# Performance work log

Measured on AMD Instinct MI355X. Metric: run time of the kernel, lower is better.

The kernel has to match this reference:

```python
import jax, jax.numpy as jnp
import numpy as np

B, T, D = 128, 2048, 256


def setup_inputs() -> dict:
    key = jax.random.key(0)
    ks = jax.random.split(key, 6)
    s = 1.0 / np.sqrt(D)  # kaiming-uniform-ish scale for bias-free Linear
    return {
        "x": jax.random.normal(ks[0], (B, T, D), jnp.float32),
        "W_in": jax.random.normal(ks[1], (D, D), jnp.float32) * s,
        "W_select": jax.random.normal(ks[2], (D, D), jnp.float32) * s,
        "W_gate": jax.random.normal(ks[3], (D, D), jnp.float32) * s,
        "W_out": jax.random.normal(ks[4], (D, D), jnp.float32) * s,
        "W_delta": jax.random.normal(ks[5], (D, D), jnp.float32) * s,
        "log_a": jnp.zeros((D,), jnp.float32),  # module inits log_a = zeros
    }


def _diag_recurrence(decay, update):
    # state_t = decay_t * state_{t-1} + update_t, state_{-1} = 0 (zero-init fast path)
    # First-order linear recurrence as an associative scan:
    # (a1,b1) o (a2,b2) = (a1*a2, a2*b1 + b2)
    def combine(c1, c2):
        a1, b1 = c1
        a2, b2 = c2
        return a1 * a2, a2 * b1 + b2

    _, states = jax.lax.associative_scan(combine, (decay, update), axis=1)
    return states  # (B, T, D)


def reference(x, W_in, W_select, W_gate, W_out, W_delta, log_a):
    # selective diag-SSM (a_mode='diag'):
    #   delta  = softplus(delta_proj(x))                  timestep / selectivity
    #   decay  = exp(-delta * exp(log_a))                 in (0, 1]
    #   update = delta * sigmoid(select_proj(x)) * in_proj(x)
    #   states = scan(state = decay*state + update)
    #   y      = states * silu(gate_proj(x)); out = out_proj(y)
    delta = jax.nn.softplus(jnp.einsum("btd,ed->bte", x, W_delta))
    decay = jnp.exp(-delta * jnp.exp(log_a))
    u = jnp.einsum("btd,ed->bte", x, W_in)
    sel = jax.nn.sigmoid(jnp.einsum("btd,ed->bte", x, W_select))
    update = delta * sel * u
    states = _diag_recurrence(decay, update)
    gate = jax.nn.silu(jnp.einsum("btd,ed->bte", x, W_gate))
    return jnp.einsum("btd,ed->bte", states * gate, W_out)
```

## Files before the change

### kernel.cpp

```cpp
#include <hip/hip_runtime.h>
#include <hip/hip_bf16.h>
#include <hip/hip_fp16.h>
#include <math.h>


typedef __attribute__((ext_vector_type(8))) short s16x8;
typedef __attribute__((ext_vector_type(4))) float f32x4;
typedef __attribute__((ext_vector_type(4))) unsigned short u16x4;

#define D_DIM 256
#define T_DIM 2048
#define B_DIM 128
#define NCHUNK 16
#define CLEN 128
#define BK 64

__device__ __forceinline__ unsigned short f2bf(float f) {
    union { float f; unsigned int u; } v; v.f = f;
    unsigned int r = v.u + 0x7fffu + ((v.u >> 16) & 1u);
    return (unsigned short)(r >> 16);
}
__device__ __forceinline__ float bf2f(unsigned short s) {
    union { unsigned int u; float f; } v; v.u = ((unsigned int)s) << 16;
    return v.f;
}
__device__ __forceinline__ void gload_lds16(const void* g, void* l) {
    __builtin_amdgcn_global_load_lds(
        (const __attribute__((address_space(1))) unsigned int*)g,
        (__attribute__((address_space(3))) unsigned int*)l, 16, 0, 0);
}

__global__ __launch_bounds__(256) void prep_kernel(
    const float* __restrict__ W_in, const float* __restrict__ W_select,
    const float* __restrict__ W_gate, const float* __restrict__ W_out,
    const float* __restrict__ W_delta, const float* __restrict__ log_a,
    unsigned short* __restrict__ Wb, float* __restrict__ ea)
{
    int i = blockIdx.x * 256 + threadIdx.x;
    if (i < 4 * 65536) {
        int row = i >> 8, k = i & 255;
        int n = row >> 2, w = row & 3;
        const float* src = (w == 0) ? W_delta : (w == 1) ? W_select
                         : (w == 2) ? W_in    : W_gate;
        Wb[i] = f2bf(src[n * 256 + k]);
    } else if (i < 5 * 65536) {
        Wb[i] = f2bf(W_out[i - 4 * 65536]);
    } else if (i < 5 * 65536 + 256) {
        int j = i - 5 * 65536;
        ea[j] = expf(log_a[j]);
    }
}

__global__ __launch_bounds__(256) void xcast_kernel(
    const float* __restrict__ x, unsigned short* __restrict__ xb)
{
    size_t i = ((size_t)blockIdx.x * 256 + threadIdx.x) * 8;
    float4 p0 = *(const float4*)(x + i);
    float4 p1 = *(const float4*)(x + i + 4);
    s16x8 a;
    a[0] = (short)f2bf(p0.x); a[1] = (short)f2bf(p0.y);
    a[2] = (short)f2bf(p0.z); a[3] = (short)f2bf(p0.w);
    a[4] = (short)f2bf(p1.x); a[5] = (short)f2bf(p1.y);
    a[6] = (short)f2bf(p1.z); a[7] = (short)f2bf(p1.w);
    *(s16x8*)(xb + i) = a;
}

__global__ __launch_bounds__(256, 3) void gemm_fused_kernel(
    const unsigned short* __restrict__ xb, const unsigned short* __restrict__ Wcat,
    const float* __restrict__ ea,
    __half2* __restrict__ du, unsigned short* __restrict__ gate)
{
    __shared__ unsigned short lds[2 * 128 * BK];
    int bid = blockIdx.x;
    int wg  = (bid & 7) * 2048 + (bid >> 3);
    int mt  = wg >> 3;
    int nt  = wg & 7;
    int mbase = mt * 128;
    int nb = nt * 128;
    int tid = threadIdx.x, lane = tid & 63, wid = tid >> 6;
    int l16 = lane & 15, lk = lane >> 4;
    int wr = wid >> 1, wc = wid & 1;
    int srow = tid >> 3;
    int sgi  = tid & 7;

    f32x4 acc[4][4] = {};

    for (int ks = 0; ks < 4; ++ks) {
        int kb = ks * BK;
#pragma unroll
        for (int j = 0; j < 4; ++j) {
            int row = j * 32 + srow;
            int sg  = sgi ^ (row & 7);
            gload_lds16(xb + (size_t)(mbase + row) * D_DIM + kb + sg * 8,
                        (char*)lds + row * 128 + sgi * 16);
        }
#pragma unroll
        for (int j = 0; j < 4; ++j) {
            int row = j * 32 + srow;
            int sg  = sgi ^ (row & 7);
            gload_lds16(Wcat + (size_t)(nb + row) * D_DIM + kb + sg * 8,
                        (char*)lds + 16384 + row * 128 + sgi * 16);
        }
        __syncthreads();

#pragma unroll
        for (int kk = 0; kk < 2; ++kk) {
            int gp = ((kk * 4 + lk) ^ (l16 & 7)) * 16;
            s16x8 xf[4], wf[4];
#pragma unroll
            for (int mf = 0; mf < 4; ++mf)
                xf[mf] = *(const s16x8*)((const char*)lds
                           + (wr * 64 + mf * 16 + l16) * 128 + gp);
#pragma unroll
            for (int nf = 0; nf < 4; ++nf)
                wf[nf] = *(const s16x8*)((const char*)lds + 16384
                           + (wc * 64 + nf * 16 + l16) * 128 + gp);
#pragma unroll
            for (int nf = 0; nf < 4; ++nf)
#pragma unroll
                for (int mf = 0; mf < 4; ++mf)
                    acc[mf][nf] = __builtin_amdgcn_mfma_f32_16x16x32_bf16(
                        wf[nf], xf[mf], acc[mf][nf], 0, 0, 0);
        }
        if (ks < 3) __syncthreads();
    }

#pragma unroll
    for (int nf = 0; nf < 4; ++nf) {
        int n = nt * 32 + wc * 16 + nf * 4 + lk;
        float ean = ea[n];
#pragma unroll
        for (int mf = 0; mf < 4; ++mf) {
            int m = mbase + wr * 64 + mf * 16 + l16;
            float zd = acc[mf][nf][0];
            float zs = acc[mf][nf][1];
            float zi = acc[mf][nf][2];
            float zg = acc[mf][nf][3];
            float e = __expf(zd);
            float delta = (zd > 15.f) ? zd : __logf(1.f + e);
            float dec = __expf(-delta * ean);
            float sel = 1.f / (1.f + __expf(-zs));
            float upd = delta * sel * zi;
            float g   = zg / (1.f + __expf(-zg));
            du[(size_t)m * D_DIM + n] = __floats2half2_rn(dec, upd);
            gate[(size_t)m * D_DIM + n] = f2bf(g);
        }
    }
}

__global__ __launch_bounds__(256) void scan1_kernel(
    const __half2* __restrict__ du,
    float* __restrict__ cA, float* __restrict__ cS)
{
    int b = blockIdx.x >> 4;
    int c = blockIdx.x & 15;
    int d = threadIdx.x;
    size_t base = ((size_t)b * T_DIM + (size_t)c * CLEN) * D_DIM + d;
    float A = 1.f, S = 0.f;
#pragma unroll 4
    for (int t = 0; t < CLEN; ++t) {
        __half2 v = du[base + (size_t)t * D_DIM];
        float dc = __low2float(v);
        float up = __high2float(v);
        A *= dc;
        S = fmaf(dc, S, up);
    }
    int idx = (b * NCHUNK + c) * D_DIM + d;
    cA[idx] = A;
    cS[idx] = S;
}

__global__ __launch_bounds__(256) void scan2_kernel(
    const float* __restrict__ cA, const float* __restrict__ cS,
    float* __restrict__ carry)
{
    int b = blockIdx.x;
    int d = threadIdx.x;
    float s = 0.f;
    for (int c = 0; c < NCHUNK; ++c) {
        int idx = (b * NCHUNK + c) * D_DIM + d;
        carry[idx] = s;
        s = fmaf(cA[idx], s, cS[idx]);
    }
}

__global__ __launch_bounds__(256) void scan_out_kernel(
    const __half2* __restrict__ du, const unsigned short* __restrict__ gate,
    const float* __restrict__ carry, const unsigned short* __restrict__ Wo,
    float* __restrict__ out)
{
    __shared__ unsigned short yls[128 * 256];
    int b = blockIdx.x >> 4;
    int c = blockIdx.x & 15;
    int tid = threadIdx.x;

    {
        int d = tid;
        size_t base = ((size_t)b * T_DIM + (size_t)c * CLEN) * D_DIM + d;
        float s = carry[(b * NCHUNK + c) * D_DIM + d];
        int dlo = d & 7, dch = d >> 3;
#pragma unroll 4
        for (int t = 0; t < CLEN; ++t) {
            __half2 v = du[base + (size_t)t * D_DIM];
            float dc = __low2float(v);
            float up = __high2float(v);
            s = fmaf(dc, s, up);
            float g = bf2f(gate[base + (size_t)t * D_DIM]);
            int off = t * 256 + ((dch ^ (t & 7)) << 3) + dlo;
            yls[off] = f2bf(s * g);
        }
    }
    __syncthreads();

    int lane = tid & 63, wid = tid >> 6;
    int l16 = lane & 15;
    int lkc = lane >> 4;
    int m0 = (wid >> 1) * 64;
    size_t rbase = (size_t)b * T_DIM + (size_t)c * CLEN;
    int r0 = lkc * 4;

    for (int nblk = 0; nblk < 2; ++nblk) {
        int n0 = (wid & 1) * 64 + nblk * 128;
        f32x4 acc[4][4] = {};
        for (int ks = 0; ks < 8; ++ks) {
            int kb = ks * 32 + lkc * 8;
            s16x8 yf[4];
#pragma unroll
            for (int mf = 0; mf < 4; ++mf) {
                int row = m0 + mf * 16 + l16;
                int chunk = (ks * 4 + lkc) ^ (row & 7);
                yf[mf] = *(const s16x8*)&yls[row * 256 + chunk * 8];
            }
#pragma unroll
            for (int nf = 0; nf < 4; ++nf) {
                s16x8 wfr = *(const s16x8*)(Wo + (size_t)(n0 + nf * 16 + l16) * D_DIM + kb);
#pragma unroll
                for (int mf = 0; mf < 4; ++mf)
                    acc[mf][nf] = __builtin_amdgcn_mfma_f32_16x16x32_bf16(
                        wfr, yf[mf], acc[mf][nf], 0, 0, 0);
            }
        }
#pragma unroll
        for (int mf = 0; mf < 4; ++mf) {
            size_t rowg = rbase + m0 + mf * 16 + l16;
#pragma unroll
            for (int nf = 0; nf < 4; ++nf) {
                int n = n0 + nf * 16 + r0;
                *(f32x4*)(out + rowg * D_DIM + n) = acc[mf][nf];
            }
        }
    }
}

extern "C" void kernel_launch(void* const* d_in, const int* in_sizes, int n_in,
                              void* d_out, int out_size, void* d_ws, size_t ws_size,
                              hipStream_t stream)
{
    const float* x        = (const float*)d_in[0];
    const float* W_in     = (const float*)d_in[1];
    const float* W_select = (const float*)d_in[2];
    const float* W_gate   = (const float*)d_in[3];
    const float* W_out    = (const float*)d_in[4];
    const float* W_delta  = (const float*)d_in[5];
    const float* log_a    = (const float*)d_in[6];
    float* out = (float*)d_out;

    char* ws = (char*)d_ws;
    const size_t MB = 1ull << 20;
    unsigned short* Wb    = (unsigned short*)(ws);
    float*          ea    = (float*)(ws + 655360);
    unsigned short* xb    = (unsigned short*)(ws + 1 * MB);
    __half2*        du    = (__half2*)(ws + 129 * MB);
    unsigned short* gate  = (unsigned short*)(ws + 385 * MB);
    float*          cA    = (float*)(ws + 513 * MB);
    float*          cS    = (float*)(ws + 515 * MB);
    float*          carry = (float*)(ws + 517 * MB);

    prep_kernel<<<1281, 256, 0, stream>>>(W_in, W_select, W_gate, W_out,
                                          W_delta, log_a, Wb, ea);
    xcast_kernel<<<32768, 256, 0, stream>>>(x, xb);
    gemm_fused_kernel<<<16384, 256, 0, stream>>>(xb, Wb, ea, du, gate);
    scan1_kernel<<<B_DIM * NCHUNK, 256, 0, stream>>>(du, cA, cS);
    scan2_kernel<<<B_DIM, 256, 0, stream>>>(cA, cS, carry);
    scan_out_kernel<<<B_DIM * NCHUNK, 256, 0, stream>>>(du, gate, carry,
                                                        Wb + 4 * 65536, out);
}
```

Measured before the change: 681.2 us.

## Keep weight panel resident in LDS and store du/gate in 16-wide panels

Each GEMM block now loads a 64-row slice of the concatenated weights into LDS once and loops over 8 M-tiles, reading x fragments straight from global memory instead of staging them through LDS. The du and gate intermediates are written in a panel-major layout of 16 channels per panel, so each block's epilogue writes contiguous 16-element runs, and the scan kernels index the same layout. This removes repeated weight staging and per-k-step barriers, at the cost of uncoalesced direct global x loads and strided scan reads across panels.

```diff
diff --git a/kernel.cpp b/kernel.cpp
--- a/kernel.cpp
+++ b/kernel.cpp
@@ -6,14 +6,14 @@
 
 typedef __attribute__((ext_vector_type(8))) short s16x8;
 typedef __attribute__((ext_vector_type(4))) float f32x4;
-typedef __attribute__((ext_vector_type(4))) unsigned short u16x4;
 
 #define D_DIM 256
 #define T_DIM 2048
 #define B_DIM 128
+#define M_DIM (B_DIM * T_DIM)
 #define NCHUNK 16
 #define CLEN 128
-#define BK 64
+#define PANEL ((size_t)M_DIM * 16)
 
 __device__ __forceinline__ unsigned short f2bf(float f) {
     union { float f; unsigned int u; } v; v.f = f;
@@ -68,98 +68,99 @@
 __global__ __launch_bounds__(256, 3) void gemm_fused_kernel(
     const unsigned short* __restrict__ xb, const unsigned short* __restrict__ Wcat,
     const float* __restrict__ ea,
-    __half2* __restrict__ du, unsigned short* __restrict__ gate)
-{
-    __shared__ unsigned short lds[2 * 128 * BK];
+    __half2* __restrict__ du_p, unsigned short* __restrict__ gate_p)
+{
+    __shared__ unsigned short wls[64 * 256];
     int bid = blockIdx.x;
-    int wg  = (bid & 7) * 2048 + (bid >> 3);
-    int mt  = wg >> 3;
-    int nt  = wg & 7;
-    int mbase = mt * 128;
-    int nb = nt * 128;
+    int wg  = (bid & 7) * 512 + (bid >> 3);
+    int nt  = wg & 15;
+    int mgrp = wg >> 4;
     int tid = threadIdx.x, lane = tid & 63, wid = tid >> 6;
     int l16 = lane & 15, lk = lane >> 4;
     int wr = wid >> 1, wc = wid & 1;
-    int srow = tid >> 3;
-    int sgi  = tid & 7;
-
-    f32x4 acc[4][4] = {};
-
-    for (int ks = 0; ks < 4; ++ks) {
-        int kb = ks * BK;
-#pragma unroll
-        for (int j = 0; j < 4; ++j) {
-            int row = j * 32 + srow;
-            int sg  = sgi ^ (row & 7);
-            gload_lds16(xb + (size_t)(mbase + row) * D_DIM + kb + sg * 8,
-                        (char*)lds + row * 128 + sgi * 16);
-        }
-#pragma unroll
-        for (int j = 0; j < 4; ++j) {
-            int row = j * 32 + srow;
-            int sg  = sgi ^ (row & 7);
-            gload_lds16(Wcat + (size_t)(nb + row) * D_DIM + kb + sg * 8,
-                        (char*)lds + 16384 + row * 128 + sgi * 16);
-        }
-        __syncthreads();
-
-#pragma unroll
-        for (int kk = 0; kk < 2; ++kk) {
-            int gp = ((kk * 4 + lk) ^ (l16 & 7)) * 16;
-            s16x8 xf[4], wf[4];
+    int nb = nt * 64;
+
+#pragma unroll
+    for (int i = 0; i < 8; ++i) {
+        int e = i * 256 + tid;
+        int r = e >> 5, gsl = e & 31;
+        int g = gsl ^ (r & 7);
+        gload_lds16(Wcat + (size_t)(nb + r) * D_DIM + g * 8,
+                    (char*)wls + r * 512 + gsl * 16);
+    }
+    __syncthreads();
+
+    float ea0 = ea[nt * 16 + wc * 8 + lk];
+    float ea1 = ea[nt * 16 + wc * 8 + 4 + lk];
+
+
+    for (int it = 0; it < 8; ++it) {
+        int mbase = (mgrp * 8 + it) * 128;
+        const unsigned short* xrow =
+            xb + (size_t)(mbase + wr * 64 + l16) * D_DIM + lk * 8;
+
+        f32x4 acc[4][2] = {};
+
+#pragma unroll
+        for (int k = 0; k < 8; ++k) {
+            s16x8 xf[4];
 #pragma unroll
             for (int mf = 0; mf < 4; ++mf)
-                xf[mf] = *(const s16x8*)((const char*)lds
-                           + (wr * 64 + mf * 16 + l16) * 128 + gp);
-#pragma unroll
-            for (int nf = 0; nf < 4; ++nf)
-                wf[nf] = *(const s16x8*)((const char*)lds + 16384
-                           + (wc * 64 + nf * 16 + l16) * 128 + gp);
-#pragma unroll
-            for (int nf = 0; nf < 4; ++nf)
+                xf[mf] = *(const s16x8*)(xrow + mf * 16 * D_DIM + k * 32);
+            s16x8 wf[2];
+#pragma unroll
+            for (int nf = 0; nf < 2; ++nf) {
+                int row = wc * 32 + nf * 16 + l16;
+                int g = (k * 4 + lk) ^ (row & 7);
+                wf[nf] = *(const s16x8*)((const char*)wls + row * 512 + g * 16);
+            }
+#pragma unroll
+            for (int nf = 0; nf < 2; ++nf)
 #pragma unroll
                 for (int mf = 0; mf < 4; ++mf)
                     acc[mf][nf] = __builtin_amdgcn_mfma_f32_16x16x32_bf16(
                         wf[nf], xf[mf], acc[mf][nf], 0, 0, 0);
         }
-        if (ks < 3) __syncthreads();
-    }
-
-#pragma unroll
-    for (int nf = 0; nf < 4; ++nf) {
-        int n = nt * 32 + wc * 16 + nf * 4 + lk;
-        float ean = ea[n];
-#pragma unroll
-        for (int mf = 0; mf < 4; ++mf) {
-            int m = mbase + wr * 64 + mf * 16 + l16;
-            float zd = acc[mf][nf][0];
-            float zs = acc[mf][nf][1];
-            float zi = acc[mf][nf][2];
-            float zg = acc[mf][nf][3];
-            float e = __expf(zd);
-            float delta = (zd > 15.f) ? zd : __logf(1.f + e);
-            float dec = __expf(-delta * ean);
-            float sel = 1.f / (1.f + __expf(-zs));
-            float upd = delta * sel * zi;
-            float g   = zg / (1.f + __expf(-zg));
-            du[(size_t)m * D_DIM + n] = __floats2half2_rn(dec, upd);
-            gate[(size_t)m * D_DIM + n] = f2bf(g);
+
+#pragma unroll
+        for (int nf = 0; nf < 2; ++nf) {
+            int n_l = wc * 8 + nf * 4 + lk;
+            float ean = nf ? ea1 : ea0;
+#pragma unroll
+            for (int mf = 0; mf < 4; ++mf) {
+                int m = mbase + wr * 64 + mf * 16 + l16;
+                float zd = acc[mf][nf][0];
+                float zs = acc[mf][nf][1];
+                float zi = acc[mf][nf][2];
+                float zg = acc[mf][nf][3];
+                float e = __expf(zd);
+                float delta = (zd > 15.f) ? zd : __logf(1.f + e);
+                float dec = __expf(-delta * ean);
+                float sel = 1.f / (1.f + __expf(-zs));
+                float upd = delta * sel * zi;
+                float g   = zg / (1.f + __expf(-zg));
+                size_t off = (size_t)nt * PANEL + (size_t)m * 16 + n_l;
+                du_p[off]   = __floats2half2_rn(dec, upd);
+                gate_p[off] = f2bf(g);
+            }
         }
     }
 }
 
 __global__ __launch_bounds__(256) void scan1_kernel(
-    const __half2* __restrict__ du,
+    const __half2* __restrict__ du_p,
     float* __restrict__ cA, float* __restrict__ cS)
 {
     int b = blockIdx.x >> 4;
     int c = blockIdx.x & 15;
     int d = threadIdx.x;
-    size_t base = ((size_t)b * T_DIM + (size_t)c * CLEN) * D_DIM + d;
+    int pan = d >> 4, off = d & 15;
+    size_t base = (size_t)pan * PANEL
+                + ((size_t)b * T_DIM + (size_t)c * CLEN) * 16 + off;
     float A = 1.f, S = 0.f;
 #pragma unroll 4
     for (int t = 0; t < CLEN; ++t) {
-        __half2 v = du[base + (size_t)t * D_DIM];
+        __half2 v = du_p[base + (size_t)t * 16];
         float dc = __low2float(v);
         float up = __high2float(v);
         A *= dc;
@@ -185,7 +186,7 @@
 }
 
 __global__ __launch_bounds__(256) void scan_out_kernel(
-    const __half2* __restrict__ du, const unsigned short* __restrict__ gate,
+    const __half2* __restrict__ du_p, const unsigned short* __restrict__ gate_p,
     const float* __restrict__ carry, const unsigned short* __restrict__ Wo,
     float* __restrict__ out)
 {
@@ -196,16 +197,19 @@
 
     {
         int d = tid;
-        size_t base = ((size_t)b * T_DIM + (size_t)c * CLEN) * D_DIM + d;
+        int pan = d >> 4, poff = d & 15;
+        size_t base = (size_t)pan * PANEL
+                    + ((size_t)b * T_DIM + (size_t)c * CLEN) * 16 + poff;
         float s = carry[(b * NCHUNK + c) * D_DIM + d];
         int dlo = d & 7, dch = d >> 3;
 #pragma unroll 4
         for (int t = 0; t < CLEN; ++t) {
-            __half2 v = du[base + (size_t)t * D_DIM];
+            size_t goff = base + (size_t)t * 16;
+            __half2 v = du_p[goff];
             float dc = __low2float(v);
             float up = __high2float(v);
             s = fmaf(dc, s, up);
-            float g = bf2f(gate[base + (size_t)t * D_DIM]);
+            float g = bf2f(gate_p[goff]);
             int off = t * 256 + ((dch ^ (t & 7)) << 3) + dlo;
             yls[off] = f2bf(s * g);
         }
@@ -279,7 +283,7 @@
     prep_kernel<<<1281, 256, 0, stream>>>(W_in, W_select, W_gate, W_out,
                                           W_delta, log_a, Wb, ea);
     xcast_kernel<<<32768, 256, 0, stream>>>(x, xb);
-    gemm_fused_kernel<<<16384, 256, 0, stream>>>(xb, Wb, ea, du, gate);
+    gemm_fused_kernel<<<4096, 256, 0, stream>>>(xb, Wb, ea, du, gate);
     scan1_kernel<<<B_DIM * NCHUNK, 256, 0, stream>>>(du, cA, cS);
     scan2_kernel<<<B_DIM, 256, 0, stream>>>(cA, cS, carry);
     scan_out_kernel<<<B_DIM * NCHUNK, 256, 0, stream>>>(du, gate, carry,
```

Measured after the change: 1.036 ms. 52.1% more time.

## Fuse chunk scan into GEMM epilogue and double-buffer LDS K-tiles

Applied to the files above, without the earlier changes.

Folds the per-chunk scan reduction (scan1) into the GEMM epilogue. Each block stages its computed (decay, update) tile in swizzled LDS, reduces it with 8 sub-segments per channel, and writes cA/cS directly, which removes a kernel launch and a full re-read of du. It also double-buffers the K-loop LDS tiles so the next tile's global loads overlap the current MFMAs. LDS use grows to 64 KB and launch bounds drop from 3 to 2 blocks per SIMD, so occupancy may fall.

```diff
diff --git a/kernel.cpp b/kernel.cpp
--- a/kernel.cpp
+++ b/kernel.cpp
@@ -6,7 +6,6 @@
 
 typedef __attribute__((ext_vector_type(8))) short s16x8;
 typedef __attribute__((ext_vector_type(4))) float f32x4;
-typedef __attribute__((ext_vector_type(4))) unsigned short u16x4;
 
 #define D_DIM 256
 #define T_DIM 2048
@@ -65,12 +64,13 @@
     *(s16x8*)(xb + i) = a;
 }
 
-__global__ __launch_bounds__(256, 3) void gemm_fused_kernel(
+__global__ __launch_bounds__(256, 2) void gemm_fused_kernel(
     const unsigned short* __restrict__ xb, const unsigned short* __restrict__ Wcat,
     const float* __restrict__ ea,
-    __half2* __restrict__ du, unsigned short* __restrict__ gate)
-{
-    __shared__ unsigned short lds[2 * 128 * BK];
+    __half2* __restrict__ du, unsigned short* __restrict__ gate,
+    float* __restrict__ cA, float* __restrict__ cS)
+{
+    __shared__ char ldsb[65536];
     int bid = blockIdx.x;
     int wg  = (bid & 7) * 2048 + (bid >> 3);
     int mt  = wg >> 3;
@@ -85,35 +85,46 @@
 
     f32x4 acc[4][4] = {};
 
-    for (int ks = 0; ks < 4; ++ks) {
-        int kb = ks * BK;
+    {
+        int kb = 0;
 #pragma unroll
         for (int j = 0; j < 4; ++j) {
             int row = j * 32 + srow;
             int sg  = sgi ^ (row & 7);
             gload_lds16(xb + (size_t)(mbase + row) * D_DIM + kb + sg * 8,
-                        (char*)lds + row * 128 + sgi * 16);
-        }
-#pragma unroll
-        for (int j = 0; j < 4; ++j) {
-            int row = j * 32 + srow;
-            int sg  = sgi ^ (row & 7);
+                        ldsb + row * 128 + sgi * 16);
             gload_lds16(Wcat + (size_t)(nb + row) * D_DIM + kb + sg * 8,
-                        (char*)lds + 16384 + row * 128 + sgi * 16);
-        }
-        __syncthreads();
-
+                        ldsb + 16384 + row * 128 + sgi * 16);
+        }
+    }
+    __syncthreads();
+
+    for (int ks = 0; ks < 4; ++ks) {
+        int bufo = (ks & 1) << 15;
+        if (ks < 3) {
+            int kb = (ks + 1) * BK;
+            int nbo = bufo ^ 32768;
+#pragma unroll
+            for (int j = 0; j < 4; ++j) {
+                int row = j * 32 + srow;
+                int sg  = sgi ^ (row & 7);
+                gload_lds16(xb + (size_t)(mbase + row) * D_DIM + kb + sg * 8,
+                            ldsb + nbo + row * 128 + sgi * 16);
+                gload_lds16(Wcat + (size_t)(nb + row) * D_DIM + kb + sg * 8,
+                            ldsb + nbo + 16384 + row * 128 + sgi * 16);
+            }
+        }
 #pragma unroll
         for (int kk = 0; kk < 2; ++kk) {
             int gp = ((kk * 4 + lk) ^ (l16 & 7)) * 16;
             s16x8 xf[4], wf[4];
 #pragma unroll
             for (int mf = 0; mf < 4; ++mf)
-                xf[mf] = *(const s16x8*)((const char*)lds
+                xf[mf] = *(const s16x8*)(ldsb + bufo
                            + (wr * 64 + mf * 16 + l16) * 128 + gp);
 #pragma unroll
             for (int nf = 0; nf < 4; ++nf)
-                wf[nf] = *(const s16x8*)((const char*)lds + 16384
+                wf[nf] = *(const s16x8*)(ldsb + bufo + 16384
                            + (wc * 64 + nf * 16 + l16) * 128 + gp);
 #pragma unroll
             for (int nf = 0; nf < 4; ++nf)
@@ -125,13 +136,18 @@
         if (ks < 3) __syncthreads();
     }
 
+    __half2* scanb = (__half2*)ldsb;
+    float2*  sums  = (float2*)(ldsb + 16384);
 #pragma unroll
     for (int nf = 0; nf < 4; ++nf) {
         int n = nt * 32 + wc * 16 + nf * 4 + lk;
         float ean = ea[n];
+        int dl = wc * 16 + nf * 4 + lk;
+        int cxor = (dl & 7) << 2;
 #pragma unroll
         for (int mf = 0; mf < 4; ++mf) {
-            int m = mbase + wr * 64 + mf * 16 + l16;
+            int t = wr * 64 + mf * 16 + l16;
+            int m = mbase + t;
             float zd = acc[mf][nf][0];
             float zs = acc[mf][nf][1];
             float zi = acc[mf][nf][2];
@@ -142,32 +158,42 @@
             float sel = 1.f / (1.f + __expf(-zs));
             float upd = delta * sel * zi;
             float g   = zg / (1.f + __expf(-zg));
-            du[(size_t)m * D_DIM + n] = __floats2half2_rn(dec, upd);
+            __half2 dv = __floats2half2_rn(dec, upd);
+            du[(size_t)m * D_DIM + n] = dv;
             gate[(size_t)m * D_DIM + n] = f2bf(g);
-        }
-    }
-}
-
-__global__ __launch_bounds__(256) void scan1_kernel(
-    const __half2* __restrict__ du,
-    float* __restrict__ cA, float* __restrict__ cS)
-{
-    int b = blockIdx.x >> 4;
-    int c = blockIdx.x & 15;
-    int d = threadIdx.x;
-    size_t base = ((size_t)b * T_DIM + (size_t)c * CLEN) * D_DIM + d;
-    float A = 1.f, S = 0.f;
+            scanb[dl * 128 + (t ^ cxor)] = dv;
+        }
+    }
+    __syncthreads();
+
+    {
+        int dloc = tid & 31, sub = tid >> 5;
+        int cxor = (dloc & 7) << 2;
+        float A = 1.f, S = 0.f;
+        int t0 = sub * 16;
 #pragma unroll 4
-    for (int t = 0; t < CLEN; ++t) {
-        __half2 v = du[base + (size_t)t * D_DIM];
-        float dc = __low2float(v);
-        float up = __high2float(v);
-        A *= dc;
-        S = fmaf(dc, S, up);
-    }
-    int idx = (b * NCHUNK + c) * D_DIM + d;
-    cA[idx] = A;
-    cS[idx] = S;
+        for (int i = 0; i < 16; ++i) {
+            int t = t0 + i;
+            __half2 v = scanb[dloc * 128 + (t ^ cxor)];
+            float dc = __low2float(v), up = __high2float(v);
+            A *= dc;
+            S = fmaf(dc, S, up);
+        }
+        sums[sub * 32 + dloc] = make_float2(A, S);
+    }
+    __syncthreads();
+    if (tid < 32) {
+        float A = 1.f, S = 0.f;
+#pragma unroll
+        for (int sub = 0; sub < 8; ++sub) {
+            float2 as = sums[sub * 32 + tid];
+            S = fmaf(as.x, S, as.y);
+            A *= as.x;
+        }
+        int idx = mt * D_DIM + nt * 32 + tid;
+        cA[idx] = A;
+        cS[idx] = S;
+    }
 }
 
 __global__ __launch_bounds__(256) void scan2_kernel(
@@ -279,8 +305,7 @@
     prep_kernel<<<1281, 256, 0, stream>>>(W_in, W_select, W_gate, W_out,
                                           W_delta, log_a, Wb, ea);
     xcast_kernel<<<32768, 256, 0, stream>>>(x, xb);
-    gemm_fused_kernel<<<16384, 256, 0, stream>>>(xb, Wb, ea, du, gate);
-    scan1_kernel<<<B_DIM * NCHUNK, 256, 0, stream>>>(du, cA, cS);
+    gemm_fused_kernel<<<16384, 256, 0, stream>>>(xb, Wb, ea, du, gate, cA, cS);
     scan2_kernel<<<B_DIM, 256, 0, stream>>>(cA, cS, carry);
     scan_out_kernel<<<B_DIM * NCHUNK, 256, 0, stream>>>(du, gate, carry,
                                                         Wb + 4 * 65536, out);
```

Measured after the change: 673.7 us. No clear change (-1.1%).

## Fuse chunk-level scan reduction into GEMM epilogue via wave shuffles

Applied to the files above, without the earlier changes.

Removes the separate scan1 pass, which re-read the whole du tensor to compute per-chunk decay products and partial sums. The GEMM epilogue now builds these aggregates in registers for its 64-row half-tile, using a cross-lane shuffle scan over the 16 lanes and a sequential combine over the 4 fragments. This gives 32 chunk summaries per batch, so scan2 iterates 32 chunks and scan_out indexes the carry at every second entry. The cost is extra shuffle and ALU work plus register pressure in the GEMM epilogue, in exchange for dropping one full read of du from global memory.

```diff
diff --git a/kernel.cpp b/kernel.cpp
--- a/kernel.cpp
+++ b/kernel.cpp
@@ -6,12 +6,11 @@
 
 typedef __attribute__((ext_vector_type(8))) short s16x8;
 typedef __attribute__((ext_vector_type(4))) float f32x4;
-typedef __attribute__((ext_vector_type(4))) unsigned short u16x4;
 
 #define D_DIM 256
 #define T_DIM 2048
 #define B_DIM 128
-#define NCHUNK 16
+#define NCHUNK2 32
 #define CLEN 128
 #define BK 64
 
@@ -68,9 +67,10 @@
 __global__ __launch_bounds__(256, 3) void gemm_fused_kernel(
     const unsigned short* __restrict__ xb, const unsigned short* __restrict__ Wcat,
     const float* __restrict__ ea,
-    __half2* __restrict__ du, unsigned short* __restrict__ gate)
-{
-    __shared__ unsigned short lds[2 * 128 * BK];
+    __half2* __restrict__ du, unsigned short* __restrict__ gate,
+    float* __restrict__ cA, float* __restrict__ cS)
+{
+    __shared__ char lds[32768];
     int bid = blockIdx.x;
     int wg  = (bid & 7) * 2048 + (bid >> 3);
     int mt  = wg >> 3;
@@ -92,14 +92,14 @@
             int row = j * 32 + srow;
             int sg  = sgi ^ (row & 7);
             gload_lds16(xb + (size_t)(mbase + row) * D_DIM + kb + sg * 8,
-                        (char*)lds + row * 128 + sgi * 16);
+                        lds + row * 128 + sgi * 16);
         }
 #pragma unroll
         for (int j = 0; j < 4; ++j) {
             int row = j * 32 + srow;
             int sg  = sgi ^ (row & 7);
             gload_lds16(Wcat + (size_t)(nb + row) * D_DIM + kb + sg * 8,
-                        (char*)lds + 16384 + row * 128 + sgi * 16);
+                        lds + 16384 + row * 128 + sgi * 16);
         }
         __syncthreads();
 
@@ -109,11 +109,11 @@
             s16x8 xf[4], wf[4];
 #pragma unroll
             for (int mf = 0; mf < 4; ++mf)
-                xf[mf] = *(const s16x8*)((const char*)lds
+                xf[mf] = *(const s16x8*)(lds
                            + (wr * 64 + mf * 16 + l16) * 128 + gp);
 #pragma unroll
             for (int nf = 0; nf < 4; ++nf)
-                wf[nf] = *(const s16x8*)((const char*)lds + 16384
+                wf[nf] = *(const s16x8*)(lds + 16384
                            + (wc * 64 + nf * 16 + l16) * 128 + gp);
 #pragma unroll
             for (int nf = 0; nf < 4; ++nf)
@@ -129,6 +129,7 @@
     for (int nf = 0; nf < 4; ++nf) {
         int n = nt * 32 + wc * 16 + nf * 4 + lk;
         float ean = ea[n];
+        float A[4], S[4];
 #pragma unroll
         for (int mf = 0; mf < 4; ++mf) {
             int m = mbase + wr * 64 + mf * 16 + l16;
@@ -144,30 +145,35 @@
             float g   = zg / (1.f + __expf(-zg));
             du[(size_t)m * D_DIM + n] = __floats2half2_rn(dec, upd);
             gate[(size_t)m * D_DIM + n] = f2bf(g);
-        }
-    }
-}
-
-__global__ __launch_bounds__(256) void scan1_kernel(
-    const __half2* __restrict__ du,
-    float* __restrict__ cA, float* __restrict__ cS)
-{
-    int b = blockIdx.x >> 4;
-    int c = blockIdx.x & 15;
-    int d = threadIdx.x;
-    size_t base = ((size_t)b * T_DIM + (size_t)c * CLEN) * D_DIM + d;
-    float A = 1.f, S = 0.f;
-#pragma unroll 4
-    for (int t = 0; t < CLEN; ++t) {
-        __half2 v = du[base + (size_t)t * D_DIM];
-        float dc = __low2float(v);
-        float up = __high2float(v);
-        A *= dc;
-        S = fmaf(dc, S, up);
-    }
-    int idx = (b * NCHUNK + c) * D_DIM + d;
-    cA[idx] = A;
-    cS[idx] = S;
+            A[mf] = dec;
+            S[mf] = upd;
+        }
+#pragma unroll
+        for (int d = 1; d < 16; d <<= 1) {
+            bool upper = (l16 & d);
+#pragma unroll
+            for (int mf = 0; mf < 4; ++mf) {
+                float Ap = __shfl_xor(A[mf], d, 64);
+                float Sp = __shfl_xor(S[mf], d, 64);
+                float Se = upper ? Sp : S[mf];
+                float Al = upper ? A[mf] : Ap;
+                float Sl = upper ? S[mf] : Sp;
+                S[mf] = fmaf(Al, Se, Sl);
+                A[mf] = A[mf] * Ap;
+            }
+        }
+        float cAe = A[0], cSe = S[0];
+#pragma unroll
+        for (int mf = 1; mf < 4; ++mf) {
+            cSe = fmaf(A[mf], cSe, S[mf]);
+            cAe *= A[mf];
+        }
+        if (l16 == 0) {
+            int hc = mt * 2 + wr;
+            cA[hc * D_DIM + n] = cAe;
+            cS[hc * D_DIM + n] = cSe;
+        }
+    }
 }
 
 __global__ __launch_bounds__(256) void scan2_kernel(
@@ -177,8 +183,8 @@
     int b = blockIdx.x;
     int d = threadIdx.x;
     float s = 0.f;
-    for (int c = 0; c < NCHUNK; ++c) {
-        int idx = (b * NCHUNK + c) * D_DIM + d;
+    for (int c = 0; c < NCHUNK2; ++c) {
+        int idx = (b * NCHUNK2 + c) * D_DIM + d;
         carry[idx] = s;
         s = fmaf(cA[idx], s, cS[idx]);
     }
@@ -197,7 +203,7 @@
     {
         int d = tid;
         size_t base = ((size_t)b * T_DIM + (size_t)c * CLEN) * D_DIM + d;
-        float s = carry[(b * NCHUNK + c) * D_DIM + d];
+        float s = carry[(b * NCHUNK2 + c * 2) * D_DIM + d];
         int dlo = d & 7, dch = d >> 3;
 #pragma unroll 4
         for (int t = 0; t < CLEN; ++t) {
@@ -273,15 +279,14 @@
     __half2*        du    = (__half2*)(ws + 129 * MB);
     unsigned short* gate  = (unsigned short*)(ws + 385 * MB);
     float*          cA    = (float*)(ws + 513 * MB);
-    float*          cS    = (float*)(ws + 515 * MB);
-    float*          carry = (float*)(ws + 517 * MB);
+    float*          cS    = (float*)(ws + 517 * MB);
+    float*          carry = (float*)(ws + 521 * MB);
 
     prep_kernel<<<1281, 256, 0, stream>>>(W_in, W_select, W_gate, W_out,
                                           W_delta, log_a, Wb, ea);
     xcast_kernel<<<32768, 256, 0, stream>>>(x, xb);
-    gemm_fused_kernel<<<16384, 256, 0, stream>>>(xb, Wb, ea, du, gate);
-    scan1_kernel<<<B_DIM * NCHUNK, 256, 0, stream>>>(du, cA, cS);
+    gemm_fused_kernel<<<16384, 256, 0, stream>>>(xb, Wb, ea, du, gate, cA, cS);
     scan2_kernel<<<B_DIM, 256, 0, stream>>>(cA, cS, carry);
-    scan_out_kernel<<<B_DIM * NCHUNK, 256, 0, stream>>>(du, gate, carry,
-                                                        Wb + 4 * 65536, out);
-}
+    scan_out_kernel<<<B_DIM * NCHUNK2 / 2, 256, 0, stream>>>(du, gate, carry,
+                                                             Wb + 4 * 65536, out);
+}
```

Result: faster. 647.3 us (-5.0%).
